# Performance work log

Hardware: AMD Instinct MI355X
Metric: run time of the kernel (lower is better)

Reference implementation:

```python
import jax, jax.numpy as jnp
import numpy as np

N = 384
C_Z = 128
N_HEADS = 4
HEAD_DIM = C_Z // N_HEADS
LN_EPS = 1e-5


def _layernorm(x, w, b):
    mu = jnp.mean(x, axis=-1, keepdims=True)
    var = jnp.mean(jnp.square(x - mu), axis=-1, keepdims=True)
    return (x - mu) * jax.lax.rsqrt(var + LN_EPS) * w + b


def setup_inputs() -> dict:
    key = jax.random.key(0)
    ks = jax.random.split(key, 6)
    z = jax.random.normal(ks[0], (N, N, C_Z), dtype=jnp.float32)
    # Linear weights stored as [in, out] (transposed vs torch) so y = x @ W + b
    qkv_w = jax.random.normal(ks[1], (C_Z, 3 * C_Z), dtype=jnp.float32) * 0.02
    qkv_b = jnp.zeros((3 * C_Z,), dtype=jnp.float32)
    out_w = jax.random.normal(ks[2], (C_Z, C_Z), dtype=jnp.float32) * 0.02
    out_b = jnp.zeros((C_Z,), dtype=jnp.float32)
    gate_w = jax.random.normal(ks[3], (C_Z, C_Z), dtype=jnp.float32) * 0.02
    gate_b = jnp.zeros((C_Z,), dtype=jnp.float32)
    ln_w = jnp.ones((C_Z,), dtype=jnp.float32)
    ln_b = jnp.zeros((C_Z,), dtype=jnp.float32)
    return {"z": z, "ln_w": ln_w, "ln_b": ln_b, "qkv_w": qkv_w, "qkv_b": qkv_b,
            "out_w": out_w, "out_b": out_b, "gate_w": gate_w, "gate_b": gate_b}


def reference(z, ln_w, ln_b, qkv_w, qkv_b, out_w, out_b, gate_w, gate_b):
    # mode == 'starting': no transpose
    z_norm = _layernorm(z, ln_w, ln_b)                      # [N, N, c_z]
    qkv = (z_norm @ qkv_w + qkv_b).reshape(N, N, 3, N_HEADS, HEAD_DIM)
    q, k, v = qkv[:, :, 0], qkv[:, :, 1], qkv[:, :, 2]      # each [N, N, h, d]
    scale = 1.0 / np.sqrt(HEAD_DIM).astype(np.float32)
    attn = jnp.einsum('inhd,jnhd->nijh', q, k) * scale      # [N, N, N, h]
    attn = jax.nn.softmax(attn, axis=1)                     # softmax over i (dim=1)
    out = jnp.einsum('nijh,jnhd->inhd', attn, v)            # [N, N, h, d]
    out = out.reshape(N, N, C_Z)
    gate = jax.nn.sigmoid(z_norm @ gate_w + gate_b)
    return z + gate * (out @ out_w + out_b)
```

## Files before the change

kernel.cpp:

```cpp
#include <hip/hip_runtime.h>
#include <hip/hip_bf16.h>

#define NN 384
#define CZ 128
#define NH 4
#define HD 32
#define MROWS (NN*NN)

typedef __hip_bfloat16 bf16;
typedef short bf16x8f __attribute__((ext_vector_type(8)));
typedef float f32x4 __attribute__((ext_vector_type(4)));
typedef unsigned short u16x8 __attribute__((ext_vector_type(8)));

__device__ __forceinline__ float b2f(unsigned short u) {
    return __uint_as_float(((unsigned)u) << 16);
}
__device__ __forceinline__ unsigned short f2b(float f) {
    unsigned u = __float_as_uint(f);
    return (unsigned short)((u + 0x7FFFu + ((u >> 16) & 1u)) >> 16);
}

__global__ __launch_bounds__(256) void ln_stats_kernel(const float* __restrict__ z,
                                                       float* __restrict__ mu,
                                                       float* __restrict__ rstd) {
    const int wave = threadIdx.x >> 6;
    const int lane = threadIdx.x & 63;
    const int r = blockIdx.x * 4 + wave;
    const float* zr = z + (size_t)r * CZ;
    float x0 = zr[lane], x1 = zr[lane + 64];
    float sum = x0 + x1;
    float sq  = x0 * x0 + x1 * x1;
    #pragma unroll
    for (int o = 32; o > 0; o >>= 1) {
        sum += __shfl_xor(sum, o, 64);
        sq  += __shfl_xor(sq,  o, 64);
    }
    if (lane == 0) {
        const float m   = sum * (1.0f / CZ);
        const float var = sq * (1.0f / CZ) - m * m;
        mu[r]   = m;
        rstd[r] = rsqrtf(var + 1e-5f);
    }
}

__global__ __launch_bounds__(256) void qkv_gemm_mfma_kernel(const float* __restrict__ z,
                                                            const float* __restrict__ mu,
                                                            const float* __restrict__ rstd,
                                                            const float* __restrict__ lnw,
                                                            const float* __restrict__ lnb,
                                                            const float* __restrict__ W,
                                                            const float* __restrict__ bias,
                                                            unsigned short* __restrict__ qkv_t) {
    __shared__ unsigned short Zt[128 * 128];

    const int tid = threadIdx.x;
    const int w = tid >> 6;
    const int l = tid & 63;
    const int col0 = blockIdx.x * 64;
    const int row0 = blockIdx.y * 128;
    const int wcol = w & 1;
    const int wrow = w >> 1;
    const int lm = l & 15;
    const int lq = l >> 4;

    #pragma unroll
    for (int it = 0; it < 8; it++) {
        const int s = it * 256 + tid;
        const int r = s >> 4;
        const int c = (s & 15) ^ (r & 7);
        const int k0 = c * 8;
        const int grow = row0 + r;
        const float m  = mu[grow];
        const float rs = rstd[grow];
        const float4 z0 = *(const float4*)(z + (size_t)grow * CZ + k0);
        const float4 z1 = *(const float4*)(z + (size_t)grow * CZ + k0 + 4);
        const float4 w0 = *(const float4*)(lnw + k0);
        const float4 w1 = *(const float4*)(lnw + k0 + 4);
        const float4 b0 = *(const float4*)(lnb + k0);
        const float4 b1 = *(const float4*)(lnb + k0 + 4);
        u16x8 pk;
        pk[0] = f2b((z0.x - m) * rs * w0.x + b0.x);
        pk[1] = f2b((z0.y - m) * rs * w0.y + b0.y);
        pk[2] = f2b((z0.z - m) * rs * w0.z + b0.z);
        pk[3] = f2b((z0.w - m) * rs * w0.w + b0.w);
        pk[4] = f2b((z1.x - m) * rs * w1.x + b1.x);
        pk[5] = f2b((z1.y - m) * rs * w1.y + b1.y);
        pk[6] = f2b((z1.z - m) * rs * w1.z + b1.z);
        pk[7] = f2b((z1.w - m) * rs * w1.w + b1.w);
        *(u16x8*)&Zt[s * 8] = pk;
    }

    bf16x8f a[2][4];
    #pragma unroll
    for (int fm = 0; fm < 2; fm++) {
        const int gcol = col0 + wcol * 32 + fm * 16 + lm;
        #pragma unroll
        for (int kk = 0; kk < 4; kk++) {
            const int kb = kk * 32 + lq * 8;
            #pragma unroll
            for (int j = 0; j < 8; j++)
                a[fm][kk][j] = (short)f2b(W[(size_t)(kb + j) * (3 * CZ) + gcol]);
        }
    }

    __syncthreads();

    f32x4 acc[2][4];
    #pragma unroll
    for (int fm = 0; fm < 2; fm++)
        #pragma unroll
        for (int fn = 0; fn < 4; fn++)
            acc[fm][fn] = (f32x4){0.0f, 0.0f, 0.0f, 0.0f};

    #pragma unroll
    for (int kk = 0; kk < 4; kk++) {
        bf16x8f bf[4];
        #pragma unroll
        for (int fn = 0; fn < 4; fn++) {
            const int r = wrow * 64 + fn * 16 + lm;
            const int ch = (kk * 4 + lq) ^ (r & 7);
            bf[fn] = *(const bf16x8f*)&Zt[(r * 16 + ch) * 8];
        }
        #pragma unroll
        for (int fm = 0; fm < 2; fm++)
            #pragma unroll
            for (int fn = 0; fn < 4; fn++)
                acc[fm][fn] = __builtin_amdgcn_mfma_f32_16x16x32_bf16(a[fm][kk], bf[fn],
                                                                      acc[fm][fn], 0, 0, 0);
    }

    #pragma unroll
    for (int fm = 0; fm < 2; fm++) {
        const int gc = col0 + wcol * 32 + fm * 16 + lq * 4;
        const float4 b4 = *(const float4*)(bias + gc);
        const int t  = gc >> 7;
        const int hh = (gc & 127) >> 5;
        const int d0 = gc & 31;
        const size_t colbase = (size_t)((t * NH + hh) * NN) * (NN * HD) + d0;
        #pragma unroll
        for (int fn = 0; fn < 4; fn++) {
            const int grow = row0 + wrow * 64 + fn * 16 + lm;
            const int i  = grow / NN;
            const int n0 = grow - i * NN;
            const size_t idx = colbase + (size_t)n0 * (NN * HD) + (size_t)i * HD;
            ushort4 pk;
            pk.x = f2b(acc[fm][fn][0] + b4.x);
            pk.y = f2b(acc[fm][fn][1] + b4.y);
            pk.z = f2b(acc[fm][fn][2] + b4.z);
            pk.w = f2b(acc[fm][fn][3] + b4.w);
            *(ushort4*)(qkv_t + idx) = pk;
        }
    }
}

__global__ __launch_bounds__(256) void attn_mfma_kernel(const unsigned short* __restrict__ qkv_t,
                                                        float* __restrict__ attn_out) {
    __shared__ unsigned short Qf[24 * 512];
    __shared__ unsigned short Kf[24 * 512];
    __shared__ unsigned short Vf[3 * 2 * 512];
    __shared__ float sst[NN];
    __shared__ unsigned short Pscr[4][16][40];

    const int b = blockIdx.x;
    const int n = b >> 2;
    const int h = b & 3;
    const int tid = threadIdx.x;
    const int w = tid >> 6;
    const int l = tid & 63;
    const int q = l >> 4;
    const int m = l & 15;
    const size_t base_q = (size_t)((0 * NH + h) * NN + n) * (NN * HD);
    const size_t base_k = (size_t)((1 * NH + h) * NN + n) * (NN * HD);
    const size_t base_v = (size_t)((2 * NH + h) * NN + n) * (NN * HD);
    const float SCALE = 0.17677669529663687f;
    const f32x4 zero = {0.0f, 0.0f, 0.0f, 0.0f};

    #pragma unroll
    for (int it = 0; it < 12; it++) {
        const int s = tid + it * 256;
        const int isK = s >= 1536;
        const int slot = isK ? (s - 1536) : s;
        const int t  = slot >> 6;
        const int l2 = slot & 63;
        const int row = t * 16 + (l2 & 15);
        const int off8 = (l2 >> 4) * 8;
        const u16x8 raw = *(const u16x8*)(qkv_t + (isK ? base_k : base_q) +
                                         (size_t)row * HD + off8);
        unsigned short* dst = (isK ? Kf : Qf) + slot * 8;
        *(u16x8*)dst = raw;
    }
    __syncthreads();

    for (int tt = 0; tt < 6; tt++) {
        const int jt = w + 4 * tt;
        const bf16x8f kb = *(const bf16x8f*)&Kf[jt * 512 + l * 8];
        float s0 = 0.f, s1 = 0.f, s2 = 0.f, s3 = 0.f;
        for (int it = 0; it < 24; it++) {
            const bf16x8f qa = *(const bf16x8f*)&Qf[it * 512 + l * 8];
            const f32x4 c = __builtin_amdgcn_mfma_f32_16x16x32_bf16(qa, kb, zero, 0, 0, 0);
            s0 += __expf(c[0] * SCALE);
            s1 += __expf(c[1] * SCALE);
            s2 += __expf(c[2] * SCALE);
            s3 += __expf(c[3] * SCALE);
        }
        float s = s0 + s1 + s2 + s3;
        s += __shfl_xor(s, 16, 64);
        s += __shfl_xor(s, 32, 64);
        if (q == 0) sst[jt * 16 + m] = 1.0f / s;
    }
    __syncthreads();

    f32x4 oacc[6][2];
    #pragma unroll
    for (int tt = 0; tt < 6; tt++) {
        oacc[tt][0] = zero;
        oacc[tt][1] = zero;
    }

    for (int vr = 0; vr < 4; vr++) {
        for (int s = tid; s < 384; s += 256) {
            const int cl = s >> 7;
            const int dh = (s >> 6) & 1;
            const int l2 = s & 63;
            const int cg = vr * 3 + cl;
            const int j0 = cg * 32 + (l2 >> 4) * 8;
            const int d  = dh * 16 + (l2 & 15);
            ushort4 pk0, pk1;
            {
                const unsigned short* vp = qkv_t + base_v + (size_t)j0 * HD + d;
                pk0.x = f2b(b2f(vp[0 * HD]) * sst[j0 + 0]);
                pk0.y = f2b(b2f(vp[1 * HD]) * sst[j0 + 1]);
                pk0.z = f2b(b2f(vp[2 * HD]) * sst[j0 + 2]);
                pk0.w = f2b(b2f(vp[3 * HD]) * sst[j0 + 3]);
                pk1.x = f2b(b2f(vp[4 * HD]) * sst[j0 + 4]);
                pk1.y = f2b(b2f(vp[5 * HD]) * sst[j0 + 5]);
                pk1.z = f2b(b2f(vp[6 * HD]) * sst[j0 + 6]);
                pk1.w = f2b(b2f(vp[7 * HD]) * sst[j0 + 7]);
            }
            unsigned short* dst = Vf + ((cl * 2 + dh) * 64 + l2) * 8;
            *(ushort4*)(dst)     = pk0;
            *(ushort4*)(dst + 4) = pk1;
        }
        __syncthreads();

        for (int cl = 0; cl < 3; cl++) {
            const int cg = vr * 3 + cl;
            const bf16x8f ka0 = *(const bf16x8f*)&Kf[(cg * 2 + 0) * 512 + l * 8];
            const bf16x8f ka1 = *(const bf16x8f*)&Kf[(cg * 2 + 1) * 512 + l * 8];
            const bf16x8f vb0 = *(const bf16x8f*)&Vf[((cl * 2 + 0) * 64 + l) * 8];
            const bf16x8f vb1 = *(const bf16x8f*)&Vf[((cl * 2 + 1) * 64 + l) * 8];
            #pragma unroll
            for (int tt = 0; tt < 6; tt++) {
                const int it = w + 4 * tt;
                const bf16x8f qb = *(const bf16x8f*)&Qf[it * 512 + l * 8];
                const f32x4 sT0 = __builtin_amdgcn_mfma_f32_16x16x32_bf16(ka0, qb, zero, 0, 0, 0);
                const f32x4 sT1 = __builtin_amdgcn_mfma_f32_16x16x32_bf16(ka1, qb, zero, 0, 0, 0);
                ushort4 p0, p1;
                p0.x = f2b(__expf(sT0[0] * SCALE));
                p0.y = f2b(__expf(sT0[1] * SCALE));
                p0.z = f2b(__expf(sT0[2] * SCALE));
                p0.w = f2b(__expf(sT0[3] * SCALE));
                p1.x = f2b(__expf(sT1[0] * SCALE));
                p1.y = f2b(__expf(sT1[1] * SCALE));
                p1.z = f2b(__expf(sT1[2] * SCALE));
                p1.w = f2b(__expf(sT1[3] * SCALE));
                *(ushort4*)&Pscr[w][m][q * 4]      = p0;
                *(ushort4*)&Pscr[w][m][16 + q * 4] = p1;
                __asm__ volatile("" ::: "memory");
                __builtin_amdgcn_s_waitcnt(0xC07F);
                const bf16x8f pa = *(const bf16x8f*)&Pscr[w][m][q * 8];
                __asm__ volatile("" ::: "memory");
                oacc[tt][0] = __builtin_amdgcn_mfma_f32_16x16x32_bf16(pa, vb0, oacc[tt][0], 0, 0, 0);
                oacc[tt][1] = __builtin_amdgcn_mfma_f32_16x16x32_bf16(pa, vb1, oacc[tt][1], 0, 0, 0);
            }
        }
        __syncthreads();
    }

    #pragma unroll
    for (int tt = 0; tt < 6; tt++) {
        const int it = w + 4 * tt;
        #pragma unroll
        for (int dt = 0; dt < 2; dt++) {
            #pragma unroll
            for (int r = 0; r < 4; r++) {
                const int i = it * 16 + q * 4 + r;
                attn_out[((size_t)i * NN + n) * CZ + h * HD + dt * 16 + m] = oacc[tt][dt][r];
            }
        }
    }
}

__global__ __launch_bounds__(256) void final_mfma_kernel(const float* __restrict__ z,
                                                         const float* __restrict__ mu,
                                                         const float* __restrict__ rstd,
                                                         const float* __restrict__ lnw,
                                                         const float* __restrict__ lnb,
                                                         const float* __restrict__ gate_w,
                                                         const float* __restrict__ gate_b,
                                                         const float* __restrict__ out_w,
                                                         const float* __restrict__ out_b,
                                                         float* out) {
    __shared__ unsigned short Zt[64 * 128];
    __shared__ unsigned short At[64 * 128];

    const int tid = threadIdx.x;
    const int w = tid >> 6;
    const int l = tid & 63;
    const int lm = l & 15;
    const int lq = l >> 4;
    const int row0 = blockIdx.x * 64;

    #pragma unroll
    for (int it = 0; it < 4; it++) {
        const int s = it * 256 + tid;
        const int r = s >> 4;
        const int c = (s & 15) ^ (r & 7);
        const int k0 = c * 8;
        const int grow = row0 + r;
        const float m  = mu[grow];
        const float rs = rstd[grow];
        const size_t gi = (size_t)grow * CZ + k0;
        const float4 z0 = *(const float4*)(z + gi);
        const float4 z1 = *(const float4*)(z + gi + 4);
        const float4 a0 = *(const float4*)(out + gi);
        const float4 a1 = *(const float4*)(out + gi + 4);
        const float4 w0 = *(const float4*)(lnw + k0);
        const float4 w1 = *(const float4*)(lnw + k0 + 4);
        const float4 b0 = *(const float4*)(lnb + k0);
        const float4 b1 = *(const float4*)(lnb + k0 + 4);
        u16x8 pz, pa;
        pz[0] = f2b((z0.x - m) * rs * w0.x + b0.x);
        pz[1] = f2b((z0.y - m) * rs * w0.y + b0.y);
        pz[2] = f2b((z0.z - m) * rs * w0.z + b0.z);
        pz[3] = f2b((z0.w - m) * rs * w0.w + b0.w);
        pz[4] = f2b((z1.x - m) * rs * w1.x + b1.x);
        pz[5] = f2b((z1.y - m) * rs * w1.y + b1.y);
        pz[6] = f2b((z1.z - m) * rs * w1.z + b1.z);
        pz[7] = f2b((z1.w - m) * rs * w1.w + b1.w);
        pa[0] = f2b(a0.x); pa[1] = f2b(a0.y); pa[2] = f2b(a0.z); pa[3] = f2b(a0.w);
        pa[4] = f2b(a1.x); pa[5] = f2b(a1.y); pa[6] = f2b(a1.z); pa[7] = f2b(a1.w);
        *(u16x8*)&Zt[s * 8] = pz;
        *(u16x8*)&At[s * 8] = pa;
    }

    bf16x8f gw[2][4], ow[2][4];
    #pragma unroll
    for (int fm = 0; fm < 2; fm++) {
        const int gcol = w * 32 + fm * 16 + lm;
        #pragma unroll
        for (int kk = 0; kk < 4; kk++) {
            const int kb = kk * 32 + lq * 8;
            #pragma unroll
            for (int j = 0; j < 8; j++) {
                gw[fm][kk][j] = (short)f2b(gate_w[(size_t)(kb + j) * CZ + gcol]);
                ow[fm][kk][j] = (short)f2b(out_w [(size_t)(kb + j) * CZ + gcol]);
            }
        }
    }

    __syncthreads();

    f32x4 acc1[2][4], acc2[2][4];
    #pragma unroll
    for (int fm = 0; fm < 2; fm++)
        #pragma unroll
        for (int fn = 0; fn < 4; fn++) {
            acc1[fm][fn] = (f32x4){0.0f, 0.0f, 0.0f, 0.0f};
            acc2[fm][fn] = (f32x4){0.0f, 0.0f, 0.0f, 0.0f};
        }

    #pragma unroll
    for (int kk = 0; kk < 4; kk++) {
        bf16x8f bz[4], ba[4];
        #pragma unroll
        for (int fn = 0; fn < 4; fn++) {
            const int r = fn * 16 + lm;
            const int ch = (kk * 4 + lq) ^ (r & 7);
            bz[fn] = *(const bf16x8f*)&Zt[(r * 16 + ch) * 8];
            ba[fn] = *(const bf16x8f*)&At[(r * 16 + ch) * 8];
        }
        #pragma unroll
        for (int fm = 0; fm < 2; fm++)
            #pragma unroll
            for (int fn = 0; fn < 4; fn++) {
                acc1[fm][fn] = __builtin_amdgcn_mfma_f32_16x16x32_bf16(gw[fm][kk], bz[fn],
                                                                       acc1[fm][fn], 0, 0, 0);
                acc2[fm][fn] = __builtin_amdgcn_mfma_f32_16x16x32_bf16(ow[fm][kk], ba[fn],
                                                                       acc2[fm][fn], 0, 0, 0);
            }
    }

    #pragma unroll
    for (int fm = 0; fm < 2; fm++) {
        const int gc = w * 32 + fm * 16 + lq * 4;
        const float4 gb4 = *(const float4*)(gate_b + gc);
        const float4 ob4 = *(const float4*)(out_b + gc);
        #pragma unroll
        for (int fn = 0; fn < 4; fn++) {
            const int grow = row0 + fn * 16 + lm;
            const size_t idx = (size_t)grow * CZ + gc;
            const float4 z4 = *(const float4*)(z + idx);
            float4 o;
            o.x = z4.x + (1.0f / (1.0f + __expf(-(acc1[fm][fn][0] + gb4.x)))) * (acc2[fm][fn][0] + ob4.x);
            o.y = z4.y + (1.0f / (1.0f + __expf(-(acc1[fm][fn][1] + gb4.y)))) * (acc2[fm][fn][1] + ob4.y);
            o.z = z4.z + (1.0f / (1.0f + __expf(-(acc1[fm][fn][2] + gb4.z)))) * (acc2[fm][fn][2] + ob4.z);
            o.w = z4.w + (1.0f / (1.0f + __expf(-(acc1[fm][fn][3] + gb4.w)))) * (acc2[fm][fn][3] + ob4.w);
            *(float4*)(out + idx) = o;
        }
    }
}

extern "C" void kernel_launch(void* const* d_in, const int* in_sizes, int n_in,
                              void* d_out, int out_size, void* d_ws, size_t ws_size,
                              hipStream_t stream) {
    const float* z      = (const float*)d_in[0];
    const float* ln_w   = (const float*)d_in[1];
    const float* ln_b   = (const float*)d_in[2];
    const float* qkv_w  = (const float*)d_in[3];
    const float* qkv_b  = (const float*)d_in[4];
    const float* out_w  = (const float*)d_in[5];
    const float* out_b  = (const float*)d_in[6];
    const float* gate_w = (const float*)d_in[7];
    const float* gate_b = (const float*)d_in[8];
    float* out = (float*)d_out;

    float* ws = (float*)d_ws;
    float* mu_buf   = ws;
    float* rstd_buf = ws + MROWS;
    unsigned short* qkv_t = (unsigned short*)(ws + 2 * MROWS);

    ln_stats_kernel<<<MROWS / 4, 256, 0, stream>>>(z, mu_buf, rstd_buf);
    qkv_gemm_mfma_kernel<<<dim3(6, MROWS / 128), 256, 0, stream>>>(z, mu_buf, rstd_buf,
                                                                   ln_w, ln_b, qkv_w, qkv_b, qkv_t);
    attn_mfma_kernel<<<NN * NH, 256, 0, stream>>>(qkv_t, out);
    final_mfma_kernel<<<MROWS / 64, 256, 0, stream>>>(z, mu_buf, rstd_buf, ln_w, ln_b,
                                                      gate_w, gate_b, out_w, out_b, out);
}
```

Baseline: 417.9 us.

## Fuse softmax column-sum pass into attention main loop, keep Q in registers

Removes the separate pass that recomputed every QK^T tile just to get the softmax denominators over i. The sums are now accumulated from the same exponentials used for P, reduced across the block per 32-column chunk, and applied to V before the PV MFMAs. Q fragments are held in registers instead of being reloaded from LDS. In exchange the kernel adds two block barriers per 32-column chunk and more register pressure (qreg and pa arrays), and P is now stored unnormalised in bf16 while V is scaled per chunk.

```diff
diff --git a/kernel.cpp b/kernel.cpp
--- a/kernel.cpp
+++ b/kernel.cpp
@@ -157,8 +157,8 @@
                                                         float* __restrict__ attn_out) {
     __shared__ unsigned short Qf[24 * 512];
     __shared__ unsigned short Kf[24 * 512];
-    __shared__ unsigned short Vf[3 * 2 * 512];
-    __shared__ float sst[NN];
+    __shared__ unsigned short Vf[2 * 64 * 8];
+    __shared__ float sred[4][32];
     __shared__ unsigned short Pscr[4][16][40];
 
     const int b = blockIdx.x;
@@ -191,24 +191,10 @@
     }
     __syncthreads();
 
-    for (int tt = 0; tt < 6; tt++) {
-        const int jt = w + 4 * tt;
-        const bf16x8f kb = *(const bf16x8f*)&Kf[jt * 512 + l * 8];
-        float s0 = 0.f, s1 = 0.f, s2 = 0.f, s3 = 0.f;
-        for (int it = 0; it < 24; it++) {
-            const bf16x8f qa = *(const bf16x8f*)&Qf[it * 512 + l * 8];
-            const f32x4 c = __builtin_amdgcn_mfma_f32_16x16x32_bf16(qa, kb, zero, 0, 0, 0);
-            s0 += __expf(c[0] * SCALE);
-            s1 += __expf(c[1] * SCALE);
-            s2 += __expf(c[2] * SCALE);
-            s3 += __expf(c[3] * SCALE);
-        }
-        float s = s0 + s1 + s2 + s3;
-        s += __shfl_xor(s, 16, 64);
-        s += __shfl_xor(s, 32, 64);
-        if (q == 0) sst[jt * 16 + m] = 1.0f / s;
-    }
-    __syncthreads();
+    bf16x8f qreg[6];
+    #pragma unroll
+    for (int tt = 0; tt < 6; tt++)
+        qreg[tt] = *(const bf16x8f*)&Qf[(w + 4 * tt) * 512 + l * 8];
 
     f32x4 oacc[6][2];
     #pragma unroll
@@ -217,64 +203,74 @@
         oacc[tt][1] = zero;
     }
 
-    for (int vr = 0; vr < 4; vr++) {
-        for (int s = tid; s < 384; s += 256) {
-            const int cl = s >> 7;
-            const int dh = (s >> 6) & 1;
-            const int l2 = s & 63;
-            const int cg = vr * 3 + cl;
-            const int j0 = cg * 32 + (l2 >> 4) * 8;
-            const int d  = dh * 16 + (l2 & 15);
-            ushort4 pk0, pk1;
-            {
-                const unsigned short* vp = qkv_t + base_v + (size_t)j0 * HD + d;
-                pk0.x = f2b(b2f(vp[0 * HD]) * sst[j0 + 0]);
-                pk0.y = f2b(b2f(vp[1 * HD]) * sst[j0 + 1]);
-                pk0.z = f2b(b2f(vp[2 * HD]) * sst[j0 + 2]);
-                pk0.w = f2b(b2f(vp[3 * HD]) * sst[j0 + 3]);
-                pk1.x = f2b(b2f(vp[4 * HD]) * sst[j0 + 4]);
-                pk1.y = f2b(b2f(vp[5 * HD]) * sst[j0 + 5]);
-                pk1.z = f2b(b2f(vp[6 * HD]) * sst[j0 + 6]);
-                pk1.w = f2b(b2f(vp[7 * HD]) * sst[j0 + 7]);
-            }
-            unsigned short* dst = Vf + ((cl * 2 + dh) * 64 + l2) * 8;
-            *(ushort4*)(dst)     = pk0;
-            *(ushort4*)(dst + 4) = pk1;
+    for (int cl = 0; cl < 12; cl++) {
+        const bf16x8f ka0 = *(const bf16x8f*)&Kf[(cl * 2 + 0) * 512 + l * 8];
+        const bf16x8f ka1 = *(const bf16x8f*)&Kf[(cl * 2 + 1) * 512 + l * 8];
+
+        float sacc[8];
+        #pragma unroll
+        for (int k = 0; k < 8; k++) sacc[k] = 0.0f;
+
+        bf16x8f pa[6];
+        #pragma unroll
+        for (int tt = 0; tt < 6; tt++) {
+            const f32x4 sT0 = __builtin_amdgcn_mfma_f32_16x16x32_bf16(ka0, qreg[tt], zero, 0, 0, 0);
+            const f32x4 sT1 = __builtin_amdgcn_mfma_f32_16x16x32_bf16(ka1, qreg[tt], zero, 0, 0, 0);
+            float p[8];
+            p[0] = __expf(sT0[0] * SCALE);
+            p[1] = __expf(sT0[1] * SCALE);
+            p[2] = __expf(sT0[2] * SCALE);
+            p[3] = __expf(sT0[3] * SCALE);
+            p[4] = __expf(sT1[0] * SCALE);
+            p[5] = __expf(sT1[1] * SCALE);
+            p[6] = __expf(sT1[2] * SCALE);
+            p[7] = __expf(sT1[3] * SCALE);
+            #pragma unroll
+            for (int k = 0; k < 8; k++) sacc[k] += p[k];
+            ushort4 p0, p1;
+            p0.x = f2b(p[0]); p0.y = f2b(p[1]); p0.z = f2b(p[2]); p0.w = f2b(p[3]);
+            p1.x = f2b(p[4]); p1.y = f2b(p[5]); p1.z = f2b(p[6]); p1.w = f2b(p[7]);
+            *(ushort4*)&Pscr[w][m][q * 4]      = p0;
+            *(ushort4*)&Pscr[w][m][16 + q * 4] = p1;
+            __asm__ volatile("" ::: "memory");
+            __builtin_amdgcn_s_waitcnt(0xC07F);
+            pa[tt] = *(const bf16x8f*)&Pscr[w][m][q * 8];
+            __asm__ volatile("" ::: "memory");
+        }
+
+        #pragma unroll
+        for (int k = 0; k < 8; k++) {
+            float v = sacc[k];
+            v += __shfl_xor(v, 1, 64);
+            v += __shfl_xor(v, 2, 64);
+            v += __shfl_xor(v, 4, 64);
+            v += __shfl_xor(v, 8, 64);
+            if (m == 0) sred[w][q * 4 + (k & 3) + (k >> 2) * 16] = v;
         }
         __syncthreads();
 
-        for (int cl = 0; cl < 3; cl++) {
-            const int cg = vr * 3 + cl;
-            const bf16x8f ka0 = *(const bf16x8f*)&Kf[(cg * 2 + 0) * 512 + l * 8];
-            const bf16x8f ka1 = *(const bf16x8f*)&Kf[(cg * 2 + 1) * 512 + l * 8];
-            const bf16x8f vb0 = *(const bf16x8f*)&Vf[((cl * 2 + 0) * 64 + l) * 8];
-            const bf16x8f vb1 = *(const bf16x8f*)&Vf[((cl * 2 + 1) * 64 + l) * 8];
-            #pragma unroll
-            for (int tt = 0; tt < 6; tt++) {
-                const int it = w + 4 * tt;
-                const bf16x8f qb = *(const bf16x8f*)&Qf[it * 512 + l * 8];
-                const f32x4 sT0 = __builtin_amdgcn_mfma_f32_16x16x32_bf16(ka0, qb, zero, 0, 0, 0);
-                const f32x4 sT1 = __builtin_amdgcn_mfma_f32_16x16x32_bf16(ka1, qb, zero, 0, 0, 0);
-                ushort4 p0, p1;
-                p0.x = f2b(__expf(sT0[0] * SCALE));
-                p0.y = f2b(__expf(sT0[1] * SCALE));
-                p0.z = f2b(__expf(sT0[2] * SCALE));
-                p0.w = f2b(__expf(sT0[3] * SCALE));
-                p1.x = f2b(__expf(sT1[0] * SCALE));
-                p1.y = f2b(__expf(sT1[1] * SCALE));
-                p1.z = f2b(__expf(sT1[2] * SCALE));
-                p1.w = f2b(__expf(sT1[3] * SCALE));
-                *(ushort4*)&Pscr[w][m][q * 4]      = p0;
-                *(ushort4*)&Pscr[w][m][16 + q * 4] = p1;
-                __asm__ volatile("" ::: "memory");
-                __builtin_amdgcn_s_waitcnt(0xC07F);
-                const bf16x8f pa = *(const bf16x8f*)&Pscr[w][m][q * 8];
-                __asm__ volatile("" ::: "memory");
-                oacc[tt][0] = __builtin_amdgcn_mfma_f32_16x16x32_bf16(pa, vb0, oacc[tt][0], 0, 0, 0);
-                oacc[tt][1] = __builtin_amdgcn_mfma_f32_16x16x32_bf16(pa, vb1, oacc[tt][1], 0, 0, 0);
-            }
+        {
+            const int jj = tid >> 3;
+            const int d0 = (tid & 7) * 4;
+            const int jg = cl * 32 + jj;
+            const ushort4 v4 = *(const ushort4*)(qkv_t + base_v + (size_t)jg * HD + d0);
+            const float inv = 1.0f / (sred[0][jj] + sred[1][jj] + sred[2][jj] + sred[3][jj]);
+            const int slotbase = (d0 >> 4) * 64 + (jj >> 3) * 16 + (d0 & 15);
+            const int e = jj & 7;
+            Vf[(slotbase + 0) * 8 + e] = f2b(b2f(v4.x) * inv);
+            Vf[(slotbase + 1) * 8 + e] = f2b(b2f(v4.y) * inv);
+            Vf[(slotbase + 2) * 8 + e] = f2b(b2f(v4.z) * inv);
+            Vf[(slotbase + 3) * 8 + e] = f2b(b2f(v4.w) * inv);
         }
         __syncthreads();
+
+        const bf16x8f vb0 = *(const bf16x8f*)&Vf[(0 * 64 + l) * 8];
+        const bf16x8f vb1 = *(const bf16x8f*)&Vf[(1 * 64 + l) * 8];
+        #pragma unroll
+        for (int tt = 0; tt < 6; tt++) {
+            oacc[tt][0] = __builtin_amdgcn_mfma_f32_16x16x32_bf16(pa[tt], vb0, oacc[tt][0], 0, 0, 0);
+            oacc[tt][1] = __builtin_amdgcn_mfma_f32_16x16x32_bf16(pa[tt], vb1, oacc[tt][1], 0, 0, 0);
+        }
     }
 
     #pragma unroll
```

Result: no change. 419.0 us (+0.3%).
